# Kernel tuning notes

Hardware: AMD Instinct MI355X
Metric: run time of the kernel (lower is better)

Reference implementation:

```python
import jax, jax.numpy as jnp
import numpy as np

LEAKY_SLOPE = 0.2  # tf.nn.leaky_relu default alpha


def setup_inputs() -> dict:
    key = jax.random.key(0)
    k1, k2, k3 = jax.random.split(key, 3)
    B, T, K, D = 64, 2048, 256, 256  # batch, timesteps, n_nodes, out_dim
    inputs = jax.random.normal(k1, (B, T, K), dtype=jnp.float32)
    W = jax.random.normal(k2, (K, D), dtype=jnp.float32) * (1.0 / np.sqrt(K))
    a = jax.random.normal(k3, (2 * D, 1), dtype=jnp.float32) * (1.0 / np.sqrt(2 * D))
    return {"inputs": inputs, "W": W, "a": a}


def reference(inputs, W, a):
    # inputs: (B, T, K); W: (K, D); a: (2D, 1)
    B, T, K = inputs.shape
    D = W.shape[1]
    H = jnp.matmul(inputs, W)  # (B, T, D)
    # Original: H_concat[b,t,k] = concat([H[b,t], H[b,t]]) for every k (both
    # repeats are of the same H), so H_concat @ a == H @ (a_i + a_j), constant in k.
    a_i = a[:D, 0]
    a_j = a[D:, 0]
    e = jax.nn.leaky_relu(H @ (a_i + a_j), negative_slope=LEAKY_SLOPE)  # (B, T)
    e = jnp.broadcast_to(e[:, :, None], (B, T, K))  # (B, T, K) -- constant along K
    alpha = jax.nn.softmax(e, axis=2)  # exactly uniform 1/K
    # sum_k alpha[b,t,k] * H[b,t,d]  (H_repeat_i[b,t,k,:] == H[b,t,:])
    H_gat = jnp.einsum('btk,btd->btd', alpha, H)  # (B, T, D)
    return H_gat
```

## Files before the change

kernel.cpp:

```cpp
#include <hip/hip_runtime.h>
#include <cstdint>


static constexpr int MTOT = 64 * 2048;
static constexpr int KDIM = 256;
static constexpr int NDIM = 256;

typedef __bf16 bf16x8 __attribute__((ext_vector_type(8)));
typedef float f32x4 __attribute__((ext_vector_type(4)));

__device__ __forceinline__ uint32_t f2bf_pk(float a, float b) {
    uint32_t ua = __float_as_uint(a);
    uint32_t ub = __float_as_uint(b);
    ua = ua + 0x7fffu + ((ua >> 16) & 1u);
    ub = ub + 0x7fffu + ((ub >> 16) & 1u);
    return (ua >> 16) | (ub & 0xffff0000u);
}

__global__ void wt_image(const float* __restrict__ W, unsigned short* __restrict__ img) {
    int k = blockIdx.x;
    int n = threadIdx.x;
    float v = W[k * NDIM + n];
    uint32_t u = __float_as_uint(v);
    u = u + 0x7fffu + ((u >> 16) & 1u);
    img[((size_t)((k >> 3) * NDIM + n) << 3) + (k & 7)] = (unsigned short)(u >> 16);
}

__global__ __launch_bounds__(1024)
void gat_gemm(const float* __restrict__ A, const uint4* __restrict__ img,
              float* __restrict__ C) {
    __shared__ uint4 Bs[8192];

    const int tid = threadIdx.x;

#pragma unroll
    for (int i = 0; i < 8; ++i)
        Bs[tid + i * 1024] = img[tid + i * 1024];

    const int lane = tid & 63;
    const int wave = tid >> 6;
    const int l15  = lane & 15;
    const int quad = lane >> 4;

    const int row = blockIdx.x * 256 + wave * 16 + l15;
    const float* arow = A + (size_t)row * KDIM;

    f32x4 acc[16];
#pragma unroll
    for (int j = 0; j < 16; ++j) acc[j] = (f32x4)0.0f;

    __syncthreads();

    float4 a0 = *(const float4*)(arow + quad * 8);
    float4 a1 = *(const float4*)(arow + quad * 8 + 4);

#pragma unroll
    for (int ks = 0; ks < 8; ++ks) {
        float4 n0, n1;
        if (ks < 7) {
            const float* p = arow + (ks + 1) * 32 + quad * 8;
            n0 = *(const float4*)(p);
            n1 = *(const float4*)(p + 4);
        }

        uint4 ap;
        ap.x = f2bf_pk(a0.x, a0.y); ap.y = f2bf_pk(a0.z, a0.w);
        ap.z = f2bf_pk(a1.x, a1.y); ap.w = f2bf_pk(a1.z, a1.w);
        bf16x8 af = __builtin_bit_cast(bf16x8, ap);

        const uint4* bbase = &Bs[(ks * 4 + quad) * 256 + l15];
#pragma unroll
        for (int j = 0; j < 16; ++j) {
            bf16x8 bf = __builtin_bit_cast(bf16x8, bbase[j * 16]);
            acc[j] = __builtin_amdgcn_mfma_f32_16x16x32_bf16(af, bf, acc[j], 0, 0, 0);
        }

        a0 = n0; a1 = n1;
    }

    const size_t rbase = (size_t)(blockIdx.x * 256 + wave * 16 + quad * 4);
#pragma unroll
    for (int j = 0; j < 16; ++j) {
        const int n = j * 16 + l15;
#pragma unroll
        for (int r = 0; r < 4; ++r)
            C[(rbase + r) * NDIM + n] = acc[j][r];
    }
}

extern "C" void kernel_launch(void* const* d_in, const int* in_sizes, int n_in,
                              void* d_out, int out_size, void* d_ws, size_t ws_size,
                              hipStream_t stream) {
    (void)in_sizes; (void)n_in; (void)out_size; (void)ws_size;
    const float* inputs = (const float*)d_in[0];
    const float* W      = (const float*)d_in[1];
    unsigned short* img = (unsigned short*)d_ws;
    float* out = (float*)d_out;

    hipLaunchKernelGGL(wt_image, dim3(KDIM), dim3(NDIM), 0, stream, W, img);
    hipLaunchKernelGGL(gat_gemm, dim3(MTOT / 256), dim3(1024), 0, stream,
                       inputs, (const uint4*)img, out);
}
```

Baseline: 247.2 us.

## Make GEMM persistent with cross-tile A prefetch and split N across wave pairs

The GEMM launches a fixed grid of 256 persistent blocks instead of one block per 256 rows. Each block loads the bf16 weight image into LDS once and loops over 128-row tiles. Each pair of waves splits the N dimension, so a wave holds 8 accumulators instead of 16. The next tile's A rows are prefetched during the current tile's MFMA steps. This amortises the per-block 128KB LDS fill of B and overlaps global loads with compute, at the cost of more live registers for the prefetched A data and fewer blocks in flight.

New measurement: 427.3 us. 72.9% more time.

```diff
diff --git a/kernel.cpp b/kernel.cpp
--- a/kernel.cpp
+++ b/kernel.cpp
@@ -2,9 +2,12 @@
 #include <cstdint>
 
 
-static constexpr int MTOT = 64 * 2048;
 static constexpr int KDIM = 256;
 static constexpr int NDIM = 256;
+static constexpr int MTOT = 131072;
+static constexpr int ROWS_PER_TILE = 128;
+static constexpr int NBLOCKS = 256;
+static constexpr int TPB = MTOT / ROWS_PER_TILE / NBLOCKS;
 
 typedef __bf16 bf16x8 __attribute__((ext_vector_type(8)));
 typedef float f32x4 __attribute__((ext_vector_type(4)));
@@ -17,6 +20,13 @@
     return (ua >> 16) | (ub & 0xffff0000u);
 }
 
+__device__ __forceinline__ uint4 pack2(float4 x, float4 y) {
+    uint4 r;
+    r.x = f2bf_pk(x.x, x.y); r.y = f2bf_pk(x.z, x.w);
+    r.z = f2bf_pk(y.x, y.y); r.w = f2bf_pk(y.z, y.w);
+    return r;
+}
+
 __global__ void wt_image(const float* __restrict__ W, unsigned short* __restrict__ img) {
     int k = blockIdx.x;
     int n = threadIdx.x;
@@ -26,66 +36,107 @@
     img[((size_t)((k >> 3) * NDIM + n) << 3) + (k & 7)] = (unsigned short)(u >> 16);
 }
 
-__global__ __launch_bounds__(1024)
+__global__ __launch_bounds__(1024, 1)
 void gat_gemm(const float* __restrict__ A, const uint4* __restrict__ img,
               float* __restrict__ C) {
     __shared__ uint4 Bs[8192];
 
-    const int tid = threadIdx.x;
+    const int tid    = threadIdx.x;
+    const int lane   = tid & 63;
+    const int wave   = tid >> 6;
+    const int l15    = lane & 15;
+    const int quad   = lane >> 4;
+    const int stripe = wave >> 1;
+    const int half   = wave & 1;
 
+    auto aptr = [&](int t) -> const float* {
+        return A + (size_t)((blockIdx.x + t * NBLOCKS) * ROWS_PER_TILE + stripe * 16 + l15) * KDIM;
+    };
+
+    float4 raw[16];
+    {
+        const float* p0 = aptr(0);
+#pragma unroll
+        for (int g = 0; g < 4; ++g) {
+            const float* p = p0 + g * 64 + quad * 8;
+            raw[g * 4 + 0] = *(const float4*)(p);
+            raw[g * 4 + 1] = *(const float4*)(p + 4);
+            raw[g * 4 + 2] = *(const float4*)(p + 32);
+            raw[g * 4 + 3] = *(const float4*)(p + 36);
+        }
+    }
 #pragma unroll
     for (int i = 0; i < 8; ++i)
         Bs[tid + i * 1024] = img[tid + i * 1024];
 
-    const int lane = tid & 63;
-    const int wave = tid >> 6;
-    const int l15  = lane & 15;
-    const int quad = lane >> 4;
+    uint4 cur[8];
+#pragma unroll
+    for (int g = 0; g < 4; ++g) {
+        cur[2 * g]     = pack2(raw[g * 4 + 0], raw[g * 4 + 1]);
+        cur[2 * g + 1] = pack2(raw[g * 4 + 2], raw[g * 4 + 3]);
+    }
 
-    const int row = blockIdx.x * 256 + wave * 16 + l15;
-    const float* arow = A + (size_t)row * KDIM;
-
-    f32x4 acc[16];
+    f32x4 acc[8];
 #pragma unroll
-    for (int j = 0; j < 16; ++j) acc[j] = (f32x4)0.0f;
+    for (int j = 0; j < 8; ++j) acc[j] = (f32x4)0.0f;
 
     __syncthreads();
 
-    float4 a0 = *(const float4*)(arow + quad * 8);
-    float4 a1 = *(const float4*)(arow + quad * 8 + 4);
-
-#pragma unroll
-    for (int ks = 0; ks < 8; ++ks) {
-        float4 n0, n1;
-        if (ks < 7) {
-            const float* p = arow + (ks + 1) * 32 + quad * 8;
-            n0 = *(const float4*)(p);
-            n1 = *(const float4*)(p + 4);
-        }
-
-        uint4 ap;
-        ap.x = f2bf_pk(a0.x, a0.y); ap.y = f2bf_pk(a0.z, a0.w);
-        ap.z = f2bf_pk(a1.x, a1.y); ap.w = f2bf_pk(a1.z, a1.w);
-        bf16x8 af = __builtin_bit_cast(bf16x8, ap);
-
-        const uint4* bbase = &Bs[(ks * 4 + quad) * 256 + l15];
-#pragma unroll
-        for (int j = 0; j < 16; ++j) {
-            bf16x8 bf = __builtin_bit_cast(bf16x8, bbase[j * 16]);
-            acc[j] = __builtin_amdgcn_mfma_f32_16x16x32_bf16(af, bf, acc[j], 0, 0, 0);
-        }
-
-        a0 = n0; a1 = n1;
+#define KSTEP(ks)                                                                 \
+    {                                                                             \
+        bf16x8 af = __builtin_bit_cast(bf16x8, cur[ks]);                          \
+        const uint4* bb = &Bs[((ks) * 4 + quad) * 256 + half * 128 + l15];        \
+        _Pragma("unroll")                                                         \
+        for (int j = 0; j < 8; ++j) {                                             \
+            bf16x8 bf = __builtin_bit_cast(bf16x8, bb[j * 16]);                   \
+            acc[j] = __builtin_amdgcn_mfma_f32_16x16x32_bf16(af, bf, acc[j], 0, 0, 0); \
+        }                                                                         \
     }
 
-    const size_t rbase = (size_t)(blockIdx.x * 256 + wave * 16 + quad * 4);
+#define LOADG(g, dst)                                                             \
+    {                                                                             \
+        const float* p = np + (g) * 64 + quad * 8;                                \
+        dst[0] = *(const float4*)(p);                                             \
+        dst[1] = *(const float4*)(p + 4);                                         \
+        dst[2] = *(const float4*)(p + 32);                                        \
+        dst[3] = *(const float4*)(p + 36);                                        \
+    }
+
+    for (int t = 0; t < TPB; ++t) {
+        const bool pf = (t < TPB - 1);
+        const float* np = pf ? aptr(t + 1) : aptr(t);
+        float4 g0[4], g1[4], g2[4], g3[4];
+
+        if (pf) LOADG(0, g0)
+        KSTEP(0)
+        if (pf) LOADG(1, g1)
+        KSTEP(1)
+        if (pf) LOADG(2, g2)
+        KSTEP(2)
+        if (pf) LOADG(3, g3)
+        KSTEP(3)
+        if (pf) { cur[0] = pack2(g0[0], g0[1]); cur[1] = pack2(g0[2], g0[3]); }
+        KSTEP(4)
+        if (pf) { cur[2] = pack2(g1[0], g1[1]); cur[3] = pack2(g1[2], g1[3]); }
+        KSTEP(5)
+        if (pf) { cur[4] = pack2(g2[0], g2[1]); cur[5] = pack2(g2[2], g2[3]); }
+        KSTEP(6)
+        KSTEP(7)
+        if (pf) { cur[6] = pack2(g3[0], g3[1]); cur[7] = pack2(g3[2], g3[3]); }
+
+        const size_t rbase = (size_t)((blockIdx.x + t * NBLOCKS) * ROWS_PER_TILE
+                                      + stripe * 16 + quad * 4);
 #pragma unroll
-    for (int j = 0; j < 16; ++j) {
-        const int n = j * 16 + l15;
+        for (int j = 0; j < 8; ++j) {
+            const int n = half * 128 + j * 16 + l15;
 #pragma unroll
-        for (int r = 0; r < 4; ++r)
-            C[(rbase + r) * NDIM + n] = acc[j][r];
+            for (int r = 0; r < 4; ++r)
+                C[(rbase + r) * NDIM + n] = acc[j][r];
+            acc[j] = (f32x4)0.0f;
+        }
     }
+#undef KSTEP
+#undef LOADG
 }
 
 extern "C" void kernel_launch(void* const* d_in, const int* in_sizes, int n_in,
@@ -98,6 +149,6 @@
     float* out = (float*)d_out;
 
     hipLaunchKernelGGL(wt_image, dim3(KDIM), dim3(NDIM), 0, stream, W, img);
-    hipLaunchKernelGGL(gat_gemm, dim3(MTOT / 256), dim3(1024), 0, stream,
+    hipLaunchKernelGGL(gat_gemm, dim3(NBLOCKS), dim3(1024), 0, stream,
                        inputs, (const uint4*)img, out);
 }
```
